# Optimization experiments

Measured on AMD Instinct MI355X. Metric: run time of the kernel, lower is better.

## Reference

```python
import jax, jax.numpy as jnp
import numpy as np

B, C, H, W = 8, 256, 64, 64
CK = 64  # C // k with k=4


def setup_inputs() -> dict:
    key = jax.random.key(0)
    ks = jax.random.split(key, 5)
    s = 1.0 / np.sqrt(C)
    return {
        "x": jax.random.normal(ks[0], (B, C, H, W), dtype=jnp.float32),
        "wq": jax.random.normal(ks[1], (CK, C), dtype=jnp.float32) * s,
        "bq": jnp.zeros((CK,), dtype=jnp.float32),
        "wk": jax.random.normal(ks[2], (CK, C), dtype=jnp.float32) * s,
        "bk": jnp.zeros((CK,), dtype=jnp.float32),
        "wv": jax.random.normal(ks[3], (C, C), dtype=jnp.float32) * s,
        "bv": jnp.zeros((C,), dtype=jnp.float32),
        "wg": jax.random.normal(ks[4], (C, C), dtype=jnp.float32) * s,
        "bg": jnp.zeros((C,), dtype=jnp.float32),
    }


def reference(x, wq, bq, wk, bk, wv, bv, wg, bg):
    b, c, h, w = x.shape
    n = h * w
    xf = x.reshape(b, c, n)  # [B, C, N]
    # 1x1 convs are channel-wise matmuls
    q = jnp.einsum('oc,bcn->bon', wq, xf) + bq[None, :, None]  # [B, Ck, N]
    k = jnp.einsum('oc,bcn->bon', wk, xf) + bk[None, :, None]  # [B, Ck, N]
    v = jnp.einsum('oc,bcn->bon', wv, xf) + bv[None, :, None]  # [B, C, N]
    # energy[b,i,j] = q[b,:,i] . k[b,:,j]
    energy = jnp.einsum('bci,bcj->bij', q, k)  # [B, N, N]
    energy = jax.nn.elu(energy) / n
    out = jnp.einsum('bcn,bnj->bcj', v, energy).reshape(b, c, h, w)
    out = jnp.einsum('oc,bchw->bohw', wg, out) + bg[None, :, None, None]
    return out
```

## Files before the change

### kernel.cpp

```cpp
#include <hip/hip_runtime.h>
#include <math.h>

#define BATCH 8
#define CH    256
#define NPIX  4096
#define CKDIM 64

typedef __attribute__((ext_vector_type(8))) short short8;
typedef __attribute__((ext_vector_type(4))) float f32x4;

#define MFMA16x16(a, b, c) __builtin_amdgcn_mfma_f32_16x16x32_bf16((a), (b), (c), 0, 0, 0)

__device__ __forceinline__ unsigned short f2bf(float f) {
    union { float f; unsigned int u; } v; v.f = f;
    unsigned int u = v.u;
    u += 0x7fffu + ((u >> 16) & 1u);
    return (unsigned short)(u >> 16);
}

__global__ void prep_kernel(const float* __restrict__ wq, const float* __restrict__ bq,
                            const float* __restrict__ wk, const float* __restrict__ bk,
                            const float* __restrict__ wv, const float* __restrict__ bv,
                            const float* __restrict__ wg,
                            unsigned short* __restrict__ W_all, float* __restrict__ bias_all) {
    int o = blockIdx.x;
    int c = threadIdx.x;
    if (o < 64) {
        W_all[o * CH + c] = f2bf(wq[o * CH + c]);
        if (c == 0) bias_all[o] = bq[o];
    } else if (o < 128) {
        int oo = o - 64;
        W_all[o * CH + c] = f2bf(wk[oo * CH + c]);
        if (c == 0) bias_all[o] = bk[oo];
    } else {
        __shared__ float wgr[CH];
        int oo = o - 128;
        wgr[c] = wg[oo * CH + c];
        __syncthreads();
        float a0 = 0.f, a1 = 0.f, a2 = 0.f, a3 = 0.f;
#pragma unroll 4
        for (int m = 0; m < CH; m += 4) {
            a0 += wgr[m + 0] * wv[(m + 0) * CH + c];
            a1 += wgr[m + 1] * wv[(m + 1) * CH + c];
            a2 += wgr[m + 2] * wv[(m + 2) * CH + c];
            a3 += wgr[m + 3] * wv[(m + 3) * CH + c];
        }
        W_all[o * CH + c] = f2bf((a0 + a1) + (a2 + a3));
        if (c == 0) {
            float b = 0.f;
            for (int m = 0; m < CH; ++m) b += wgr[m] * bv[m];
            bias_all[o] = b;
        }
    }
}

__global__ __launch_bounds__(256, 2)
void qkvf_mfma(const float* __restrict__ x,
               const unsigned short* __restrict__ W_all,
               const float* __restrict__ bias_all,
               unsigned short* __restrict__ qk, unsigned short* __restrict__ vp) {
    __shared__ float Tl[64][65];
    __shared__ __align__(16) unsigned short Xl[64][264];

    int n0   = blockIdx.x * 64;
    int b    = blockIdx.y;
    int tid  = threadIdx.x;
    int lane = tid & 63;
    int w    = tid >> 6;
    int col  = lane & 15;
    int quad = lane >> 4;

    for (int c0 = 0; c0 < CH; c0 += 64) {
        if (c0) __syncthreads();
#pragma unroll
        for (int r = 0; r < 4; ++r) {
            int f  = r * 256 + tid;
            int c  = f >> 4;
            int n4 = f & 15;
            float4 v = *(const float4*)(x + ((size_t)b * CH + c0 + c) * NPIX + n0 + n4 * 4);
            Tl[n4 * 4 + 0][c] = v.x;
            Tl[n4 * 4 + 1][c] = v.y;
            Tl[n4 * 4 + 2][c] = v.z;
            Tl[n4 * 4 + 3][c] = v.w;
        }
        __syncthreads();
#pragma unroll
        for (int r = 0; r < 2; ++r) {
            int f    = r * 256 + tid;
            int nrow = f >> 3;
            int c8   = f & 7;
            unsigned int pk[4];
#pragma unroll
            for (int p = 0; p < 4; ++p) {
                unsigned int lo = f2bf(Tl[nrow][c8 * 8 + p * 2 + 0]);
                unsigned int hi = f2bf(Tl[nrow][c8 * 8 + p * 2 + 1]);
                pk[p] = lo | (hi << 16);
            }
            *(uint4*)&Xl[nrow][c0 + c8 * 8] = *(uint4*)pk;
        }
    }
    __syncthreads();

#pragma unroll
    for (int og = 0; og < 6; ++og) {
        int o0 = og * 64;
        const unsigned short* Arow = W_all + (size_t)(o0 + w * 16 + col) * CH + quad * 8;

        f32x4 acc[4];
#pragma unroll
        for (int t = 0; t < 4; ++t) acc[t] = (f32x4){0.f, 0.f, 0.f, 0.f};

#pragma unroll
        for (int kc = 0; kc < 8; ++kc) {
            short8 a = *(const short8*)(Arow + kc * 32);
#pragma unroll
            for (int nt = 0; nt < 4; ++nt) {
                short8 bb = *(const short8*)&Xl[nt * 16 + col][kc * 32 + quad * 8];
                acc[nt] = MFMA16x16(a, bb, acc[nt]);
            }
        }

        float4 bias = *(const float4*)(bias_all + o0 + w * 16 + quad * 4);
        float bs[4] = {bias.x, bias.y, bias.z, bias.w};

        if (og < 2) {
#pragma unroll
            for (int nt = 0; nt < 4; ++nt) {
                int n = n0 + nt * 16 + col;
                unsigned int pk[2];
#pragma unroll
                for (int p = 0; p < 2; ++p) {
                    unsigned int lo = f2bf(acc[nt][p * 2 + 0] + bs[p * 2 + 0]);
                    unsigned int hi = f2bf(acc[nt][p * 2 + 1] + bs[p * 2 + 1]);
                    pk[p] = lo | (hi << 16);
                }
                *(uint2*)(qk + ((size_t)b * NPIX + n) * 128 + o0 + w * 16 + quad * 4) = *(uint2*)pk;
            }
        } else {
#pragma unroll
            for (int nt = 0; nt < 4; ++nt) {
                int n = n0 + nt * 16 + col;
#pragma unroll
                for (int r = 0; r < 4; ++r) {
                    int oo = o0 - 128 + w * 16 + quad * 4 + r;
                    vp[((size_t)b * CH + oo) * NPIX + n] = f2bf(acc[nt][r] + bs[r]);
                }
            }
        }
    }
}

#define LPK 72
__global__ __launch_bounds__(512, 4)
void attn_v6(const unsigned short* __restrict__ qk,
             const unsigned short* __restrict__ vp,
             const float* __restrict__ bg, float* __restrict__ out) {
    __shared__ __align__(16) unsigned short Qt[64][LPK];
    __shared__ __align__(16) unsigned short St[64][LPK];

    int lin  = blockIdx.y * gridDim.x + blockIdx.x;
    int b    = lin & 7;
    int j0   = (lin >> 3) * 64;
    int tid  = threadIdx.x;
    int lane = tid & 63;
    int w    = tid >> 6;
    int col  = lane & 15;
    int quad = lane >> 4;

    int tjA = w & 3;
    int tiP = (w >> 2) * 2;

    short8 bK[2];
#pragma unroll
    for (int ks = 0; ks < 2; ++ks)
        bK[ks] = *(const short8*)(qk + ((size_t)b * NPIX + j0 + tjA * 16 + col) * 128 + 64 + ks * 32 + quad * 8);

    f32x4 acc[2][4];
#pragma unroll
    for (int ot = 0; ot < 2; ++ot)
#pragma unroll
        for (int tj = 0; tj < 4; ++tj) acc[ot][tj] = (f32x4){0.f, 0.f, 0.f, 0.f};

    int qrow = tid >> 3, q8 = tid & 7;
    const unsigned short* Qsrc = qk + ((size_t)b * NPIX + qrow) * 128 + q8 * 8;
    const unsigned short* Vsrc[2];
#pragma unroll
    for (int ot = 0; ot < 2; ++ot)
        Vsrc[ot] = vp + ((size_t)b * CH + (w * 2 + ot) * 16 + col) * NPIX + quad * 8;

    uint4 qr = *(const uint4*)Qsrc;
    short8 vb[2][2];
#pragma unroll
    for (int ot = 0; ot < 2; ++ot)
#pragma unroll
        for (int ks = 0; ks < 2; ++ks)
            vb[ot][ks] = *(const short8*)(Vsrc[ot] + ks * 32);

    const float invN = 1.f / (float)NPIX;

    for (int i0 = 0; i0 < NPIX; i0 += 64) {
        *(uint4*)&Qt[qrow][q8 * 8] = qr;

        int inext = (i0 + 64) & (NPIX - 1);
        uint4 qr_n = *(const uint4*)(Qsrc + (size_t)inext * 128);
        short8 vb_n[2][2];
#pragma unroll
        for (int ot = 0; ot < 2; ++ot)
#pragma unroll
            for (int ks = 0; ks < 2; ++ks)
                vb_n[ot][ks] = *(const short8*)(Vsrc[ot] + inext + ks * 32);

        __syncthreads();

#pragma unroll
        for (int t = 0; t < 2; ++t) {
            int ti = tiP + t;
            short8 a0 = *(const short8*)&Qt[ti * 16 + col][quad * 8];
            short8 a1 = *(const short8*)&Qt[ti * 16 + col][32 + quad * 8];
            f32x4 s = (f32x4){0.f, 0.f, 0.f, 0.f};
            s = MFMA16x16(a0, bK[0], s);
            s = MFMA16x16(a1, bK[1], s);
            unsigned int pk2[2];
#pragma unroll
            for (int pp = 0; pp < 2; ++pp) {
                float e0 = s[pp * 2 + 0];
                float e1 = s[pp * 2 + 1];
                float g0 = __expf(e0) - 1.f;
                float g1 = __expf(e1) - 1.f;
                e0 = (e0 > 0.f) ? e0 : g0;
                e1 = (e1 > 0.f) ? e1 : g1;
                e0 *= invN;
                e1 *= invN;
                unsigned int rpk;
                asm("v_cvt_pk_bf16_f32 %0, %1, %2" : "=v"(rpk) : "v"(e0), "v"(e1));
                pk2[pp] = rpk;
            }
            *(uint2*)&St[tjA * 16 + col][ti * 16 + quad * 4] = *(uint2*)pk2;
        }
        __syncthreads();

#pragma unroll
        for (int ks = 0; ks < 2; ++ks) {
            short8 sb[4];
#pragma unroll
            for (int tj = 0; tj < 4; ++tj)
                sb[tj] = *(const short8*)&St[tj * 16 + col][ks * 32 + quad * 8];
            __builtin_amdgcn_s_setprio(1);
#pragma unroll
            for (int ot = 0; ot < 2; ++ot)
#pragma unroll
                for (int tj = 0; tj < 4; ++tj)
                    acc[ot][tj] = MFMA16x16(sb[tj], vb[ot][ks], acc[ot][tj]);
            __builtin_amdgcn_s_setprio(0);
        }

        qr = qr_n;
#pragma unroll
        for (int ot = 0; ot < 2; ++ot)
#pragma unroll
            for (int ks = 0; ks < 2; ++ks)
                vb[ot][ks] = vb_n[ot][ks];
    }

#pragma unroll
    for (int ot = 0; ot < 2; ++ot) {
        int o = (w * 2 + ot) * 16 + col;
        float bgv = bg[o];
#pragma unroll
        for (int tj = 0; tj < 4; ++tj) {
            int j = j0 + tj * 16 + quad * 4;
            float4 st;
            st.x = acc[ot][tj][0] + bgv;
            st.y = acc[ot][tj][1] + bgv;
            st.z = acc[ot][tj][2] + bgv;
            st.w = acc[ot][tj][3] + bgv;
            *(float4*)&out[((size_t)b * CH + o) * NPIX + j] = st;
        }
    }
}

extern "C" void kernel_launch(void* const* d_in, const int* in_sizes, int n_in,
                              void* d_out, int out_size, void* d_ws, size_t ws_size,
                              hipStream_t stream) {
    const float* x  = (const float*)d_in[0];
    const float* wq = (const float*)d_in[1];
    const float* bq = (const float*)d_in[2];
    const float* wk = (const float*)d_in[3];
    const float* bk = (const float*)d_in[4];
    const float* wv = (const float*)d_in[5];
    const float* bv = (const float*)d_in[6];
    const float* wg = (const float*)d_in[7];
    const float* bg = (const float*)d_in[8];
    float* out = (float*)d_out;

    unsigned short* W_all = (unsigned short*)d_ws;
    float* bias_all = (float*)(W_all + 384 * 256);
    unsigned short* qk = (unsigned short*)(bias_all + 384);
    unsigned short* vp = qk + (size_t)BATCH * NPIX * 128;

    prep_kernel<<<dim3(384), dim3(256), 0, stream>>>(wq, bq, wk, bk, wv, bv, wg, W_all, bias_all);
    qkvf_mfma<<<dim3(NPIX / 64, BATCH), dim3(256), 0, stream>>>(x, W_all, bias_all, qk, vp);
    attn_v6<<<dim3(NPIX / 64, BATCH), dim3(512), 0, stream>>>(qk, vp, bg, out);
}
```

Before: 257.5 us.

## Software-pipeline attention loop with double-buffered Q and S tiles, one barrier per iteration

Restructures the attention kernel's main loop so the S·V MFMA for the previous tile runs in the same phase as the Q·K energy computation for the current tile. Qt and St are double-buffered in shared memory, which removes one of the two __syncthreads per iteration and adds a prologue and an epilogue. The aim is to overlap the ELU/exp work with the MFMA accumulate and cut barrier stalls. In exchange it doubles LDS use, which may lower occupancy, and it may increase register pressure.

```diff
diff --git a/kernel.cpp b/kernel.cpp
--- a/kernel.cpp
+++ b/kernel.cpp
@@ -152,11 +152,11 @@
 
 #define LPK 72
 __global__ __launch_bounds__(512, 4)
-void attn_v6(const unsigned short* __restrict__ qk,
-             const unsigned short* __restrict__ vp,
-             const float* __restrict__ bg, float* __restrict__ out) {
-    __shared__ __align__(16) unsigned short Qt[64][LPK];
-    __shared__ __align__(16) unsigned short St[64][LPK];
+void attn_v11(const unsigned short* __restrict__ qk,
+              const unsigned short* __restrict__ vp,
+              const float* __restrict__ bg, float* __restrict__ out) {
+    __shared__ __align__(16) unsigned short Qt[2][64][LPK];
+    __shared__ __align__(16) unsigned short St[2][64][LPK];
 
     int lin  = blockIdx.y * gridDim.x + blockIdx.x;
     int b    = lin & 7;
@@ -188,7 +188,13 @@
     for (int ot = 0; ot < 2; ++ot)
         Vsrc[ot] = vp + ((size_t)b * CH + (w * 2 + ot) * 16 + col) * NPIX + quad * 8;
 
-    uint4 qr = *(const uint4*)Qsrc;
+    const float invN = 1.f / (float)NPIX;
+
+    {
+        uint4 q0 = *(const uint4*)Qsrc;
+        *(uint4*)&Qt[0][qrow][q8 * 8] = q0;
+    }
+    uint4 qrA = *(const uint4*)(Qsrc + (size_t)64 * 128);
     short8 vb[2][2];
 #pragma unroll
     for (int ot = 0; ot < 2; ++ot)
@@ -196,27 +202,75 @@
         for (int ks = 0; ks < 2; ++ks)
             vb[ot][ks] = *(const short8*)(Vsrc[ot] + ks * 32);
 
-    const float invN = 1.f / (float)NPIX;
-
-    for (int i0 = 0; i0 < NPIX; i0 += 64) {
-        *(uint4*)&Qt[qrow][q8 * 8] = qr;
-
-        int inext = (i0 + 64) & (NPIX - 1);
-        uint4 qr_n = *(const uint4*)(Qsrc + (size_t)inext * 128);
+    __syncthreads();
+
+#pragma unroll
+    for (int t = 0; t < 2; ++t) {
+        int ti = tiP + t;
+        short8 a0 = *(const short8*)&Qt[0][ti * 16 + col][quad * 8];
+        short8 a1 = *(const short8*)&Qt[0][ti * 16 + col][32 + quad * 8];
+        f32x4 s = (f32x4){0.f, 0.f, 0.f, 0.f};
+        s = MFMA16x16(a0, bK[0], s);
+        s = MFMA16x16(a1, bK[1], s);
+        unsigned int pk2[2];
+#pragma unroll
+        for (int pp = 0; pp < 2; ++pp) {
+            float e0 = s[pp * 2 + 0];
+            float e1 = s[pp * 2 + 1];
+            float g0 = __expf(e0) - 1.f;
+            float g1 = __expf(e1) - 1.f;
+            e0 = (e0 > 0.f) ? e0 : g0;
+            e1 = (e1 > 0.f) ? e1 : g1;
+            e0 *= invN;
+            e1 *= invN;
+            unsigned int rpk;
+            asm("v_cvt_pk_bf16_f32 %0, %1, %2" : "=v"(rpk) : "v"(e0), "v"(e1));
+            pk2[pp] = rpk;
+        }
+        *(uint2*)&St[0][tjA * 16 + col][ti * 16 + quad * 4] = *(uint2*)pk2;
+    }
+    *(uint4*)&Qt[1][qrow][q8 * 8] = qrA;
+    qrA = *(const uint4*)(Qsrc + (size_t)(2 * 64) * 128);
+
+    for (int it = 1; it < NPIX / 64; ++it) {
+        int pw = it & 1;
+
+        __syncthreads();
+
+        *(uint4*)&Qt[pw ^ 1][qrow][q8 * 8] = qrA;
+
+        {
+            size_t iq = (size_t)(((it + 2) * 64) & (NPIX - 1));
+            qrA = *(const uint4*)(Qsrc + iq * 128);
+        }
+        int iv = it * 64;
         short8 vb_n[2][2];
 #pragma unroll
         for (int ot = 0; ot < 2; ++ot)
 #pragma unroll
             for (int ks = 0; ks < 2; ++ks)
-                vb_n[ot][ks] = *(const short8*)(Vsrc[ot] + inext + ks * 32);
-
-        __syncthreads();
+                vb_n[ot][ks] = *(const short8*)(Vsrc[ot] + iv + ks * 32);
+
+#pragma unroll
+        for (int ks = 0; ks < 2; ++ks) {
+            short8 sb[4];
+#pragma unroll
+            for (int tj = 0; tj < 4; ++tj)
+                sb[tj] = *(const short8*)&St[pw ^ 1][tj * 16 + col][ks * 32 + quad * 8];
+            __builtin_amdgcn_s_setprio(1);
+#pragma unroll
+            for (int ot = 0; ot < 2; ++ot)
+#pragma unroll
+                for (int tj = 0; tj < 4; ++tj)
+                    acc[ot][tj] = MFMA16x16(sb[tj], vb[ot][ks], acc[ot][tj]);
+            __builtin_amdgcn_s_setprio(0);
+        }
 
 #pragma unroll
         for (int t = 0; t < 2; ++t) {
             int ti = tiP + t;
-            short8 a0 = *(const short8*)&Qt[ti * 16 + col][quad * 8];
-            short8 a1 = *(const short8*)&Qt[ti * 16 + col][32 + quad * 8];
+            short8 a0 = *(const short8*)&Qt[pw][ti * 16 + col][quad * 8];
+            short8 a1 = *(const short8*)&Qt[pw][ti * 16 + col][32 + quad * 8];
             f32x4 s = (f32x4){0.f, 0.f, 0.f, 0.f};
             s = MFMA16x16(a0, bK[0], s);
             s = MFMA16x16(a1, bK[1], s);
@@ -235,31 +289,28 @@
                 asm("v_cvt_pk_bf16_f32 %0, %1, %2" : "=v"(rpk) : "v"(e0), "v"(e1));
                 pk2[pp] = rpk;
             }
-            *(uint2*)&St[tjA * 16 + col][ti * 16 + quad * 4] = *(uint2*)pk2;
-        }
-        __syncthreads();
-
-#pragma unroll
-        for (int ks = 0; ks < 2; ++ks) {
-            short8 sb[4];
-#pragma unroll
-            for (int tj = 0; tj < 4; ++tj)
-                sb[tj] = *(const short8*)&St[tj * 16 + col][ks * 32 + quad * 8];
-            __builtin_amdgcn_s_setprio(1);
-#pragma unroll
-            for (int ot = 0; ot < 2; ++ot)
-#pragma unroll
-                for (int tj = 0; tj < 4; ++tj)
-                    acc[ot][tj] = MFMA16x16(sb[tj], vb[ot][ks], acc[ot][tj]);
-            __builtin_amdgcn_s_setprio(0);
-        }
-
-        qr = qr_n;
+            *(uint2*)&St[pw][tjA * 16 + col][ti * 16 + quad * 4] = *(uint2*)pk2;
+        }
+
 #pragma unroll
         for (int ot = 0; ot < 2; ++ot)
 #pragma unroll
             for (int ks = 0; ks < 2; ++ks)
                 vb[ot][ks] = vb_n[ot][ks];
+    }
+
+    __syncthreads();
+#pragma unroll
+    for (int ks = 0; ks < 2; ++ks) {
+        short8 sb[4];
+#pragma unroll
+        for (int tj = 0; tj < 4; ++tj)
+            sb[tj] = *(const short8*)&St[1][tj * 16 + col][ks * 32 + quad * 8];
+#pragma unroll
+        for (int ot = 0; ot < 2; ++ot)
+#pragma unroll
+            for (int tj = 0; tj < 4; ++tj)
+                acc[ot][tj] = MFMA16x16(sb[tj], vb[ot][ks], acc[ot][tj]);
     }
 
 #pragma unroll
@@ -300,5 +351,5 @@
 
     prep_kernel<<<dim3(384), dim3(256), 0, stream>>>(wq, bq, wk, bk, wv, bv, wg, W_all, bias_all);
     qkvf_mfma<<<dim3(NPIX / 64, BATCH), dim3(256), 0, stream>>>(x, W_all, bias_all, qk, vp);
-    attn_v6<<<dim3(NPIX / 64, BATCH), dim3(512), 0, stream>>>(qk, vp, bg, out);
-}
+    attn_v11<<<dim3(NPIX / 64, BATCH), dim3(512), 0, stream>>>(qk, vp, bg, out);
+}
```

Result: no change. 256.1 us (-0.5%).
